# Kernel optimization log

Hardware: AMD Instinct MI355X
Metric: run time of the kernel (lower is better)

The kernel has to match this reference:

```python
import jax, jax.numpy as jnp
import numpy as np

N = 100000   # nodes
E = 1600000  # edges (avg degree 16)
IN = 24
HID = 128
OUT = 12


def setup_inputs() -> dict:
    key = jax.random.key(0)
    ks = jax.random.split(key, 16)
    s = 0.05
    return {
        "inputs": jax.random.normal(ks[0], (N, IN), jnp.float32),
        "src": jax.random.randint(ks[1], (E,), 0, N),
        "dst": jax.random.randint(ks[2], (E,), 0, N),
        "e_w": jax.random.uniform(ks[3], (E, 1), jnp.float32),
        "snorm_n": jax.random.uniform(ks[4], (N, 1), jnp.float32),
        "snorm_e": jax.random.uniform(ks[5], (E, 1), jnp.float32),
        "W_emb": jax.random.normal(ks[6], (IN, HID), jnp.float32) * s,
        "b_emb": jnp.zeros((HID,), jnp.float32),
        "W_self1": jax.random.normal(ks[7], (HID, HID), jnp.float32) * s,
        "W1": jax.random.normal(ks[8], (HID, HID), jnp.float32) * s,
        "b1": jnp.zeros((HID,), jnp.float32),
        "W_self2": jax.random.normal(ks[9], (HID, HID), jnp.float32) * s,
        "W2": jax.random.normal(ks[10], (HID, HID), jnp.float32) * s,
        "b2": jnp.zeros((HID,), jnp.float32),
        "W_fc": jax.random.normal(ks[11], (HID, OUT), jnp.float32) * s,
        "b_fc": jnp.zeros((OUT,), jnp.float32),
    }


def _degrees(src, dst):
    out_deg = jnp.clip(jnp.zeros((N,), jnp.float32).at[src].add(1.0), 1.0)
    in_deg = jnp.clip(jnp.zeros((N,), jnp.float32).at[dst].add(1.0), 1.0)
    return out_deg, in_deg


def _gcn_layer(h, src, dst, e_w, out_deg, in_deg, W_self, W, b):
    # self transform (no bias)
    h_s = h @ W_self
    # source-side symmetric norm, edge-weighted message, sum-aggregate at dst
    feat = h * (out_deg ** -0.5)[:, None]          # [N, H]
    m = feat[src] * e_w                            # [E, H]  u_mul_e
    agg = jax.ops.segment_sum(m, dst, num_segments=N)  # [N, H] sum reduce
    h2 = (agg @ W + b) * (in_deg ** -0.5)[:, None]
    return h_s + h2


def reference(inputs, src, dst, e_w, snorm_n, snorm_e,
              W_emb, b_emb, W_self1, W1, b1, W_self2, W2, b2, W_fc, b_fc):
    out_deg, in_deg = _degrees(src, dst)
    h = inputs @ W_emb + b_emb
    h = jax.nn.relu(_gcn_layer(h, src, dst, e_w, out_deg, in_deg, W_self1, W1, b1))
    h = jax.nn.relu(_gcn_layer(h, src, dst, e_w, out_deg, in_deg, W_self2, W2, b2))
    return h @ W_fc + b_fc
```

## Files before the change

### kernel.cpp

```cpp
#include <hip/hip_runtime.h>

#define NN 100000
#define EE 1600000
#define IN_F 24
#define HID 128
#define OUT_F 12
#define LBLK 128

#define NBKT 782
#define PA_BLKS 512
#define PA_EPB 3125

#define EMB_B 2048
#define PREP_B 264
#define K1_GRID (PA_BLKS + EMB_B + PREP_B)

typedef unsigned char u8;
typedef unsigned short u16;
typedef unsigned int u32;

using short8 = __attribute__((ext_vector_type(8))) short;
using f32x4  = __attribute__((ext_vector_type(4))) float;

__device__ __forceinline__ float bf2f(u16 h) {
  return __uint_as_float(((u32)h) << 16);
}
__device__ __forceinline__ u16 f2bf(float f) {
  u32 u = __float_as_uint(f);
  u32 r = (u + 0x7FFFu + ((u >> 16) & 1u)) >> 16;
  return (u16)r;
}
__device__ __forceinline__ float inv_sqrt_cnt(int c) {
  if (c < 1) c = 1;
  return 1.0f / sqrtf((float)c);
}

__device__ __forceinline__ void emb_body(int eb, const float* __restrict__ inputs,
                                         const float* __restrict__ W_emb,
                                         const float* __restrict__ b_emb,
                                         u16* __restrict__ harr, float* smemW) {
  int t = threadIdx.x;
  float* Wls = smemW;
  float* bls = smemW + IN_F * HID;
  for (int i = t; i < IN_F * HID; i += 256) Wls[i] = W_emb[i];
  if (t < HID) bls[t] = b_emb[t];
  __syncthreads();
  int c = t & 127;
  int sub = t >> 7;
  for (int node = eb * 2 + sub; node < NN; node += EMB_B * 2) {
    const float* xr = inputs + (size_t)node * IN_F;
    float acc = bls[c];
    #pragma unroll
    for (int k = 0; k < IN_F; ++k) acc = fmaf(xr[k], Wls[k * HID + c], acc);
    harr[(size_t)node * HID + c] = f2bf(acc);
  }
}

__device__ __forceinline__ void prep_body(int pb,
    const float* __restrict__ Ws1, const float* __restrict__ W1m,
    const float* __restrict__ Ws2, const float* __restrict__ W2m,
    const float* __restrict__ Wfc,
    u16* __restrict__ WT1, u16* __restrict__ WT2, u16* __restrict__ WfcT) {
  int idx = pb * 256 + (int)threadIdx.x;
  if (idx < 65536) {
    int layer = idx >> 15;
    int rem = idx & 32767;
    int n = rem >> 8, k = rem & 255;
    const float* A = layer ? Ws2 : Ws1;
    const float* B = layer ? W2m : W1m;
    float v = (k < HID) ? A[(size_t)k * HID + n] : B[(size_t)(k - HID) * HID + n];
    (layer ? WT2 : WT1)[(size_t)n * 256 + k] = f2bf(v);
  } else if (idx < 65536 + 2048) {
    int j = idx - 65536;
    int n = j >> 7, k = j & 127;
    WfcT[(size_t)n * 128 + k] = f2bf(n < OUT_F ? Wfc[(size_t)k * OUT_F + n] : 0.f);
  }
}

__global__ __launch_bounds__(256) void k1(
    const int* __restrict__ src, const int* __restrict__ dst,
    u32* __restrict__ histgD, u32* __restrict__ histgS,
    const float* __restrict__ inputs, const float* __restrict__ W_emb,
    const float* __restrict__ b_emb, u16* __restrict__ harr,
    const float* __restrict__ Ws1, const float* __restrict__ W1m,
    const float* __restrict__ Ws2, const float* __restrict__ W2m,
    const float* __restrict__ Wfc,
    u16* __restrict__ WT1, u16* __restrict__ WT2, u16* __restrict__ WfcT) {
  __shared__ __align__(16) char sm[13312];
  int b = blockIdx.x, t = threadIdx.x;
  if (b < PA_BLKS) {
    u32* histD = (u32*)sm;
    u32* histS = histD + 1024;
    for (int i = t; i < 2048; i += 256) histD[i] = 0;
    __syncthreads();
    int e0 = b * PA_EPB;
    for (int e = e0 + t; e < e0 + PA_EPB; e += 256) {
      atomicAdd(&histD[dst[e] >> 7], 1u);
      atomicAdd(&histS[src[e] >> 7], 1u);
    }
    __syncthreads();
    for (int i = t; i < 1024; i += 256) {
      histgD[(size_t)b * 1024 + i] = histD[i];
      histgS[(size_t)b * 1024 + i] = histS[i];
    }
  } else if (b < PA_BLKS + EMB_B) {
    emb_body(b - PA_BLKS, inputs, W_emb, b_emb, harr, (float*)sm);
  } else {
    prep_body(b - PA_BLKS - EMB_B, Ws1, W1m, Ws2, W2m, Wfc, WT1, WT2, WfcT);
  }
}

__global__ __launch_bounds__(256) void k_scan1(u32* __restrict__ histgD,
                                               u32* __restrict__ histgS,
                                               u32* __restrict__ totalsD,
                                               u32* __restrict__ totalsS) {
  __shared__ u32 s[512];
  int b = blockIdx.x, t = threadIdx.x;
  u32* hist = (b < NBKT) ? histgD : histgS;
  u32* tot  = (b < NBKT) ? totalsD : totalsS;
  int k = (b < NBKT) ? b : b - NBKT;
  u32 v0 = hist[(size_t)t * 1024 + k];
  u32 v1 = hist[(size_t)(t + 256) * 1024 + k];
  s[t] = v0; s[t + 256] = v1;
  __syncthreads();
  for (int off = 1; off < 512; off <<= 1) {
    u32 a0 = (t >= off) ? s[t - off] : 0;
    u32 a1 = (t + 256 >= off) ? s[t + 256 - off] : 0;
    __syncthreads();
    s[t] += a0; s[t + 256] += a1;
    __syncthreads();
  }
  hist[(size_t)t * 1024 + k] = s[t] - v0;
  hist[(size_t)(t + 256) * 1024 + k] = s[t + 256] - v1;
  if (t == 255) tot[k] = s[511];
}

__global__ __launch_bounds__(1024) void k_scan2(const u32* __restrict__ totalsD,
                                                const u32* __restrict__ totalsS,
                                                u32* __restrict__ estartD,
                                                u32* __restrict__ sstart) {
  __shared__ u32 s[1024];
  const u32* tot = blockIdx.x ? totalsS : totalsD;
  u32* est       = blockIdx.x ? sstart  : estartD;
  int t = threadIdx.x;
  u32 v = (t < NBKT) ? tot[t] : 0;
  s[t] = v;
  __syncthreads();
  for (int off = 1; off < 1024; off <<= 1) {
    u32 a = (t >= off) ? s[t - off] : 0;
    __syncthreads();
    s[t] += a;
    __syncthreads();
  }
  if (t < NBKT) est[t] = s[t] - v;
  if (t == NBKT - 1) est[NBKT] = s[t];
}

__global__ __launch_bounds__(256) void k_passbS(
    const int* __restrict__ src, const u32* __restrict__ histgS,
    const u32* __restrict__ sstart, u8* __restrict__ lo8) {
  __shared__ u32 cur[1024];
  int pb = blockIdx.x, t = threadIdx.x;
  for (int i = t; i < 1024; i += 256)
    cur[i] = ((i < NBKT) ? sstart[i] : 0u) + histgS[(size_t)pb * 1024 + i];
  __syncthreads();
  int e0 = pb * PA_EPB;
  for (int e = e0 + t; e < e0 + PA_EPB; e += 256) {
    int s = src[e];
    u32 pos = atomicAdd(&cur[s >> 7], 1u);
    lo8[pos] = (u8)(s & 127);
  }
}

__global__ __launch_bounds__(256) void k_countS(const u8* __restrict__ lo8,
                                                const u32* __restrict__ sstart,
                                                float* __restrict__ out_norm) {
  __shared__ u32 cnt[128];
  int k = blockIdx.x, t = threadIdx.x;
  if (t < 128) cnt[t] = 0;
  __syncthreads();
  int e0 = (int)sstart[k], e1 = (int)sstart[k + 1];
  for (int e = e0 + t; e < e1; e += 256) atomicAdd(&cnt[lo8[e]], 1u);
  __syncthreads();
  if (t < 128) {
    int node = k * 128 + t;
    if (node < NN) out_norm[node] = inv_sqrt_cnt((int)cnt[t]);
  }
}

__global__ __launch_bounds__(256) void k_passbD(
    const int* __restrict__ src, const int* __restrict__ dst,
    const float* __restrict__ e_w, const float* __restrict__ out_norm,
    const u32* __restrict__ histgD, const u32* __restrict__ estartD,
    u32* __restrict__ csr_stage, u8* __restrict__ dl8) {
  __shared__ u32 cur[1024];
  int pb = blockIdx.x, t = threadIdx.x;
  for (int i = t; i < 1024; i += 256)
    cur[i] = ((i < NBKT) ? estartD[i] : 0u) + histgD[(size_t)pb * 1024 + i];
  __syncthreads();
  int e0 = pb * PA_EPB;
  for (int e = e0 + t; e < e0 + PA_EPB; e += 256) {
    int s = src[e], d = dst[e];
    float w = e_w[e] * out_norm[s];
    u32 pos = atomicAdd(&cur[d >> 7], 1u);
    csr_stage[pos] = (((u32)f2bf(w)) << 17) | (u32)s;
    dl8[pos] = (u8)(d & 127);
  }
}

__global__ __launch_bounds__(256) void k_reorder(
    const u32* __restrict__ csr_stage, const u8* __restrict__ dl8,
    const u32* __restrict__ estart, u32* __restrict__ csr,
    int* __restrict__ row_start, float* __restrict__ in_norm) {
  __shared__ u32 cnt[128], pfx[128], cur[128];
  int k = blockIdx.x, t = threadIdx.x;
  if (t < 128) cnt[t] = 0;
  __syncthreads();
  int e0 = (int)estart[k], e1 = (int)estart[k + 1];
  for (int e = e0 + t; e < e1; e += 256) atomicAdd(&cnt[dl8[e]], 1u);
  __syncthreads();
  if (t < 128) pfx[t] = cnt[t];
  __syncthreads();
  for (int off = 1; off < 128; off <<= 1) {
    u32 v = (t < 128 && t >= off) ? pfx[t - off] : 0;
    __syncthreads();
    if (t < 128) pfx[t] += v;
    __syncthreads();
  }
  if (t < 128) {
    u32 start = (u32)e0 + pfx[t] - cnt[t];
    cur[t] = start;
    int node = k * 128 + t;
    if (node < NN) {
      row_start[node] = (int)start;
      in_norm[node] = inv_sqrt_cnt((int)cnt[t]);
    }
  }
  if (k == NBKT - 1 && t == 0) row_start[NN] = e1;
  __syncthreads();
  for (int e = e0 + t; e < e1; e += 256) {
    u32 pos = atomicAdd(&cur[dl8[e]], 1u);
    csr[pos] = csr_stage[e];
  }
}

__global__ __launch_bounds__(256) void k_agg(const u16* __restrict__ harr,
                                             const int* __restrict__ row_start,
                                             const float* __restrict__ in_norm,
                                             const u32* __restrict__ csr,
                                             u16* __restrict__ aggr) {
  int t = threadIdx.x;
  int node = blockIdx.x * 8 + (t >> 5);
  if (node >= NN) return;
  int lane = t & 31;
  int s0 = row_start[node], s1 = row_start[node + 1];
  float ax = 0.f, ay = 0.f, az = 0.f, aw = 0.f;
  for (int i0 = s0; i0 < s1; i0 += 32) {
    u32 pk = 0;
    if (i0 + lane < s1) pk = csr[i0 + lane];
    int m = s1 - i0; if (m > 32) m = 32;
    int j = 0;
    for (; j + 4 <= m; j += 4) {
      u32 p0 = __shfl(pk, j,     32);
      u32 p1 = __shfl(pk, j + 1, 32);
      u32 p2 = __shfl(pk, j + 2, 32);
      u32 p3 = __shfl(pk, j + 3, 32);
      ushort4 h0 = *(const ushort4*)(harr + (size_t)(p0 & 0x1FFFF) * HID + lane * 4);
      ushort4 h1 = *(const ushort4*)(harr + (size_t)(p1 & 0x1FFFF) * HID + lane * 4);
      ushort4 h2 = *(const ushort4*)(harr + (size_t)(p2 & 0x1FFFF) * HID + lane * 4);
      ushort4 h3 = *(const ushort4*)(harr + (size_t)(p3 & 0x1FFFF) * HID + lane * 4);
      float w0 = bf2f((u16)(p0 >> 17));
      float w1 = bf2f((u16)(p1 >> 17));
      float w2 = bf2f((u16)(p2 >> 17));
      float w3 = bf2f((u16)(p3 >> 17));
      ax = fmaf(w0, bf2f(h0.x), ax); ay = fmaf(w0, bf2f(h0.y), ay);
      az = fmaf(w0, bf2f(h0.z), az); aw = fmaf(w0, bf2f(h0.w), aw);
      ax = fmaf(w1, bf2f(h1.x), ax); ay = fmaf(w1, bf2f(h1.y), ay);
      az = fmaf(w1, bf2f(h1.z), az); aw = fmaf(w1, bf2f(h1.w), aw);
      ax = fmaf(w2, bf2f(h2.x), ax); ay = fmaf(w2, bf2f(h2.y), ay);
      az = fmaf(w2, bf2f(h2.z), az); aw = fmaf(w2, bf2f(h2.w), aw);
      ax = fmaf(w3, bf2f(h3.x), ax); ay = fmaf(w3, bf2f(h3.y), ay);
      az = fmaf(w3, bf2f(h3.z), az); aw = fmaf(w3, bf2f(h3.w), aw);
    }
    for (; j < m; ++j) {
      u32 p = __shfl(pk, j, 32);
      float w = bf2f((u16)(p >> 17));
      ushort4 hv = *(const ushort4*)(harr + (size_t)(p & 0x1FFFF) * HID + lane * 4);
      ax = fmaf(w, bf2f(hv.x), ax); ay = fmaf(w, bf2f(hv.y), ay);
      az = fmaf(w, bf2f(hv.z), az); aw = fmaf(w, bf2f(hv.w), aw);
    }
  }
  float inn = in_norm[node];
  ushort4 r;
  r.x = f2bf(ax * inn); r.y = f2bf(ay * inn);
  r.z = f2bf(az * inn); r.w = f2bf(aw * inn);
  *(ushort4*)(aggr + (size_t)node * HID + lane * 4) = r;
}

template<int FC>
__global__ __launch_bounds__(512) void k_layer(u16* __restrict__ harr,
    const u16* __restrict__ aggr,
    const u16* __restrict__ WT, const float* __restrict__ bias,
    const float* __restrict__ in_norm,
    const u16* __restrict__ WfcT, const float* __restrict__ b_fc,
    float* __restrict__ out) {
  __shared__ char smem[135168];
  const int t = threadIdx.x;
  const int r0 = blockIdx.x * LBLK;

  #pragma unroll
  for (int i = 0; i < 4; ++i) {
    int boff = i * 8192 + t * 16;
    int row = boff >> 8, col = boff & 255;
    uint4 v = *(const uint4*)(harr + (size_t)(r0 + row) * HID + (col >> 1));
    *(uint4*)(smem + row * 512 + (col ^ ((row & 7) << 4))) = v;
  }
  #pragma unroll
  for (int i = 0; i < 4; ++i) {
    int boff = i * 8192 + t * 16;
    int row = boff >> 8, col = boff & 255;
    uint4 v = *(const uint4*)(aggr + (size_t)(r0 + row) * HID + (col >> 1));
    *(uint4*)(smem + row * 512 + (256 + (col ^ ((row & 7) << 4)))) = v;
  }
  #pragma unroll
  for (int i = 0; i < 8; ++i) {
    int boff = i * 8192 + t * 16;
    int row = boff >> 9, col = boff & 511;
    uint4 v = *(const uint4*)(WT + (size_t)row * 256 + (col >> 1));
    *(uint4*)(smem + 65536 + row * 512 + (col ^ ((row & 7) << 4))) = v;
  }
  if (FC && t < 256) {
    int row = t >> 4, col = (t & 15) * 16;
    uint4 v = *(const uint4*)(WfcT + (size_t)row * 128 + (col >> 1));
    *(uint4*)(smem + 131072 + row * 256 + (col ^ ((row & 7) << 4))) = v;
  }
  __syncthreads();

  const int lane = t & 63, w = t >> 6;
  const int l15 = lane & 15, lhi = lane >> 4;

  f32x4 acc[8];
  #pragma unroll
  for (int nf = 0; nf < 8; ++nf) acc[nf] = (f32x4){0.f, 0.f, 0.f, 0.f};

  const int arow = w * 16 + l15;
  const char* pa = smem + arow * 512;
  const int aswz = (arow & 7) << 4;
  #pragma unroll
  for (int ks = 0; ks < 8; ++ks) {
    int kb = ks * 64 + (lhi << 4);
    short8 a = *(const short8*)(pa + (kb ^ aswz));
    #pragma unroll
    for (int nf = 0; nf < 8; ++nf) {
      int brow = nf * 16 + l15;
      short8 bf = *(const short8*)(smem + 65536 + brow * 512 + (kb ^ ((brow & 7) << 4)));
      acc[nf] = __builtin_amdgcn_mfma_f32_16x16x32_bf16(a, bf, acc[nf], 0, 0, 0);
    }
  }

  float bcol[8];
  #pragma unroll
  for (int nf = 0; nf < 8; ++nf) bcol[nf] = bias[nf * 16 + l15];

  if (!FC) {
    #pragma unroll
    for (int r = 0; r < 4; ++r) {
      int grow = r0 + w * 16 + (lhi << 2) + r;
      if (grow < NN) {
        float inn = in_norm[grow];
        #pragma unroll
        for (int nf = 0; nf < 8; ++nf) {
          float v = acc[nf][r] + inn * bcol[nf];
          harr[(size_t)grow * HID + nf * 16 + l15] = f2bf(fmaxf(v, 0.f));
        }
      }
    }
  } else {
    #pragma unroll
    for (int r = 0; r < 4; ++r) {
      int lrow = w * 16 + (lhi << 2) + r;
      int grow = r0 + lrow;
      float inn = (grow < NN) ? in_norm[grow] : 0.f;
      #pragma unroll
      for (int nf = 0; nf < 8; ++nf) {
        int col = nf * 16 + l15;
        float v = fmaxf(acc[nf][r] + inn * bcol[nf], 0.f);
        *(u16*)(smem + lrow * 256 + ((col * 2) ^ ((lrow & 7) << 4))) = f2bf(v);
      }
    }
    __syncthreads();
    f32x4 a2 = (f32x4){0.f, 0.f, 0.f, 0.f};
    const char* pa2 = smem + (w * 16 + l15) * 256;
    const int as2 = (l15 & 7) << 4;
    #pragma unroll
    for (int ks = 0; ks < 4; ++ks) {
      int kb = ks * 64 + (lhi << 4);
      short8 a = *(const short8*)(pa2 + (kb ^ as2));
      short8 bf = *(const short8*)(smem + 131072 + l15 * 256 + (kb ^ as2));
      a2 = __builtin_amdgcn_mfma_f32_16x16x32_bf16(a, bf, a2, 0, 0, 0);
    }
    if (l15 < OUT_F) {
      float bo = b_fc[l15];
      #pragma unroll
      for (int r = 0; r < 4; ++r) {
        int grow = r0 + w * 16 + (lhi << 2) + r;
        if (grow < NN) out[(size_t)grow * OUT_F + l15] = a2[r] + bo;
      }
    }
  }
}

extern "C" void kernel_launch(void* const* d_in, const int* in_sizes, int n_in,
                              void* d_out, int out_size, void* d_ws, size_t ws_size,
                              hipStream_t stream) {
  (void)in_sizes; (void)n_in; (void)out_size;
  const float* inputs  = (const float*)d_in[0];
  const int*   src     = (const int*)d_in[1];
  const int*   dst     = (const int*)d_in[2];
  const float* e_w     = (const float*)d_in[3];
  const float* W_emb   = (const float*)d_in[6];
  const float* b_emb   = (const float*)d_in[7];
  const float* W_self1 = (const float*)d_in[8];
  const float* W1      = (const float*)d_in[9];
  const float* b1      = (const float*)d_in[10];
  const float* W_self2 = (const float*)d_in[11];
  const float* W2      = (const float*)d_in[12];
  const float* b2      = (const float*)d_in[13];
  const float* W_fc    = (const float*)d_in[14];
  const float* b_fc    = (const float*)d_in[15];
  float* out = (float*)d_out;

  u32* histgD      = (u32*)d_ws;
  u32* histgS      = histgD + (size_t)512 * 1024;
  u32* totalsD     = histgS + (size_t)512 * 1024;
  u32* estartD     = totalsD + 1024;
  u32* totalsS     = estartD + 1024;
  u32* sstart      = totalsS + 1024;
  float* out_norm  = (float*)(sstart + 1024);
  float* in_norm   = out_norm + NN;
  int* row_start   = (int*)(in_norm + NN);
  u8* lo8          = (u8*)(row_start + NN + 4);
  u32* csr_stage   = (u32*)(lo8 + EE);
  u32* csr         = csr_stage + EE;
  u16* harr        = (u16*)(csr + EE);
  u16* aggr        = harr + (size_t)NN * HID;
  u16* WT1         = aggr + (size_t)NN * HID;
  u16* WT2         = WT1 + 32768;
  u16* WfcT        = WT2 + 32768;

  const size_t NEED = (size_t)2 * 512 * 1024 * 4 + 4096 * 4 + (size_t)(3 * NN + 4) * 4
                      + (size_t)EE * 9 + (size_t)NN * HID * 4 + (2 * 32768 + 2048) * 2;
  if (ws_size < NEED) return;

  hipLaunchKernelGGL(k1, dim3(K1_GRID), dim3(256), 0, stream,
                     src, dst, histgD, histgS, inputs, W_emb, b_emb, harr,
                     W_self1, W1, W_self2, W2, W_fc, WT1, WT2, WfcT);
  hipLaunchKernelGGL(k_scan1, dim3(2 * NBKT), dim3(256), 0, stream,
                     histgD, histgS, totalsD, totalsS);
  hipLaunchKernelGGL(k_scan2, dim3(2), dim3(1024), 0, stream,
                     totalsD, totalsS, estartD, sstart);
  hipLaunchKernelGGL(k_passbS, dim3(PA_BLKS), dim3(256), 0, stream,
                     src, histgS, sstart, lo8);
  hipLaunchKernelGGL(k_countS, dim3(NBKT), dim3(256), 0, stream, lo8, sstart, out_norm);
  hipLaunchKernelGGL(k_passbD, dim3(PA_BLKS), dim3(256), 0, stream,
                     src, dst, e_w, out_norm, histgD, estartD, csr_stage, lo8);
  hipLaunchKernelGGL(k_reorder, dim3(NBKT), dim3(256), 0, stream,
                     csr_stage, lo8, estartD, csr, row_start, in_norm);
  hipLaunchKernelGGL(k_agg, dim3((NN + 7) / 8), dim3(256), 0, stream,
                     harr, row_start, in_norm, csr, aggr);
  hipLaunchKernelGGL(k_layer<0>, dim3((NN + LBLK - 1) / LBLK), dim3(512), 0, stream,
                     harr, aggr, WT1, b1, in_norm, WfcT, b_fc, out);
  hipLaunchKernelGGL(k_agg, dim3((NN + 7) / 8), dim3(256), 0, stream,
                     harr, row_start, in_norm, csr, aggr);
  hipLaunchKernelGGL(k_layer<1>, dim3((NN + LBLK - 1) / LBLK), dim3(512), 0, stream,
                     harr, aggr, WT2, b2, in_norm, WfcT, b_fc, out);
}
```

Before: 352.8 us.

## Merge src/dst bucket passes and widen aggregation loads to 16 bytes

The separate source and destination bucketing passes become one kernel that reads src/dst once and scatters into both bucket arrays. Because out_norm is no longer known during bucketing, the out-degree norm is applied later in the aggregation kernel, where each edge weight is rescaled on load. The aggregation kernel now has each half-warp load 8 bf16 values (16 bytes) per lane and handle alternating edges, combining the halves with a shuffle at the end. This saves a launch and a pass over the edge arrays, at the cost of extra norm gathers and bf16 re-rounding in both aggregation calls. It also adds a barrier in the layer kernel and reuses the csr buffer as temporary space for the source bytes.

```diff
diff --git a/kernel.cpp b/kernel.cpp
--- a/kernel.cpp
+++ b/kernel.cpp
@@ -30,6 +30,8 @@
   u32 r = (u + 0x7FFFu + ((u >> 16) & 1u)) >> 16;
   return (u16)r;
 }
+__device__ __forceinline__ float bflo(u32 p) { return __uint_as_float(p << 16); }
+__device__ __forceinline__ float bfhi(u32 p) { return __uint_as_float(p & 0xFFFF0000u); }
 __device__ __forceinline__ float inv_sqrt_cnt(int c) {
   if (c < 1) c = 1;
   return 1.0f / sqrtf((float)c);
@@ -156,23 +158,31 @@
   if (t == NBKT - 1) est[NBKT] = s[t];
 }
 
-__global__ __launch_bounds__(256) void k_passbS(
-    const int* __restrict__ src, const u32* __restrict__ histgS,
-    const u32* __restrict__ sstart, u8* __restrict__ lo8) {
-  __shared__ u32 cur[1024];
+__global__ __launch_bounds__(256) void k_passb(
+    const int* __restrict__ src, const int* __restrict__ dst,
+    const float* __restrict__ e_w,
+    const u32* __restrict__ histgD, const u32* __restrict__ estartD,
+    const u32* __restrict__ histgS, const u32* __restrict__ sstart,
+    u32* __restrict__ csr_stage, u8* __restrict__ dl8, u8* __restrict__ sl8) {
+  __shared__ u32 curD[1024], curS[1024];
   int pb = blockIdx.x, t = threadIdx.x;
-  for (int i = t; i < 1024; i += 256)
-    cur[i] = ((i < NBKT) ? sstart[i] : 0u) + histgS[(size_t)pb * 1024 + i];
+  for (int i = t; i < 1024; i += 256) {
+    curD[i] = ((i < NBKT) ? estartD[i] : 0u) + histgD[(size_t)pb * 1024 + i];
+    curS[i] = ((i < NBKT) ? sstart[i] : 0u) + histgS[(size_t)pb * 1024 + i];
+  }
   __syncthreads();
   int e0 = pb * PA_EPB;
   for (int e = e0 + t; e < e0 + PA_EPB; e += 256) {
-    int s = src[e];
-    u32 pos = atomicAdd(&cur[s >> 7], 1u);
-    lo8[pos] = (u8)(s & 127);
-  }
-}
-
-__global__ __launch_bounds__(256) void k_countS(const u8* __restrict__ lo8,
+    int s = src[e], d = dst[e];
+    u32 posS = atomicAdd(&curS[s >> 7], 1u);
+    sl8[posS] = (u8)(s & 127);
+    u32 posD = atomicAdd(&curD[d >> 7], 1u);
+    csr_stage[posD] = (((u32)f2bf(e_w[e])) << 17) | (u32)s;
+    dl8[posD] = (u8)(d & 127);
+  }
+}
+
+__global__ __launch_bounds__(256) void k_countS(const u8* __restrict__ sl8,
                                                 const u32* __restrict__ sstart,
                                                 float* __restrict__ out_norm) {
   __shared__ u32 cnt[128];
@@ -180,31 +190,11 @@
   if (t < 128) cnt[t] = 0;
   __syncthreads();
   int e0 = (int)sstart[k], e1 = (int)sstart[k + 1];
-  for (int e = e0 + t; e < e1; e += 256) atomicAdd(&cnt[lo8[e]], 1u);
+  for (int e = e0 + t; e < e1; e += 256) atomicAdd(&cnt[sl8[e]], 1u);
   __syncthreads();
   if (t < 128) {
     int node = k * 128 + t;
     if (node < NN) out_norm[node] = inv_sqrt_cnt((int)cnt[t]);
-  }
-}
-
-__global__ __launch_bounds__(256) void k_passbD(
-    const int* __restrict__ src, const int* __restrict__ dst,
-    const float* __restrict__ e_w, const float* __restrict__ out_norm,
-    const u32* __restrict__ histgD, const u32* __restrict__ estartD,
-    u32* __restrict__ csr_stage, u8* __restrict__ dl8) {
-  __shared__ u32 cur[1024];
-  int pb = blockIdx.x, t = threadIdx.x;
-  for (int i = t; i < 1024; i += 256)
-    cur[i] = ((i < NBKT) ? estartD[i] : 0u) + histgD[(size_t)pb * 1024 + i];
-  __syncthreads();
-  int e0 = pb * PA_EPB;
-  for (int e = e0 + t; e < e0 + PA_EPB; e += 256) {
-    int s = src[e], d = dst[e];
-    float w = e_w[e] * out_norm[s];
-    u32 pos = atomicAdd(&cur[d >> 7], 1u);
-    csr_stage[pos] = (((u32)f2bf(w)) << 17) | (u32)s;
-    dl8[pos] = (u8)(d & 127);
   }
 }
 
@@ -247,54 +237,72 @@
 __global__ __launch_bounds__(256) void k_agg(const u16* __restrict__ harr,
                                              const int* __restrict__ row_start,
                                              const float* __restrict__ in_norm,
+                                             const float* __restrict__ out_norm,
                                              const u32* __restrict__ csr,
                                              u16* __restrict__ aggr) {
   int t = threadIdx.x;
   int node = blockIdx.x * 8 + (t >> 5);
   if (node >= NN) return;
   int lane = t & 31;
+  int half = lane >> 4;
+  int li = lane & 15;
   int s0 = row_start[node], s1 = row_start[node + 1];
-  float ax = 0.f, ay = 0.f, az = 0.f, aw = 0.f;
+  float acc[8] = {0.f, 0.f, 0.f, 0.f, 0.f, 0.f, 0.f, 0.f};
   for (int i0 = s0; i0 < s1; i0 += 32) {
-    u32 pk = 0;
-    if (i0 + lane < s1) pk = csr[i0 + lane];
+    u32 pk2 = 0;
+    if (i0 + lane < s1) {
+      u32 pk = csr[i0 + lane];
+      u32 sv = pk & 0x1FFFF;
+      float w = bf2f((u16)(pk >> 17)) * out_norm[sv];
+      pk2 = (((u32)f2bf(w)) << 17) | sv;
+    }
     int m = s1 - i0; if (m > 32) m = 32;
-    int j = 0;
-    for (; j + 4 <= m; j += 4) {
-      u32 p0 = __shfl(pk, j,     32);
-      u32 p1 = __shfl(pk, j + 1, 32);
-      u32 p2 = __shfl(pk, j + 2, 32);
-      u32 p3 = __shfl(pk, j + 3, 32);
-      ushort4 h0 = *(const ushort4*)(harr + (size_t)(p0 & 0x1FFFF) * HID + lane * 4);
-      ushort4 h1 = *(const ushort4*)(harr + (size_t)(p1 & 0x1FFFF) * HID + lane * 4);
-      ushort4 h2 = *(const ushort4*)(harr + (size_t)(p2 & 0x1FFFF) * HID + lane * 4);
-      ushort4 h3 = *(const ushort4*)(harr + (size_t)(p3 & 0x1FFFF) * HID + lane * 4);
-      float w0 = bf2f((u16)(p0 >> 17));
-      float w1 = bf2f((u16)(p1 >> 17));
-      float w2 = bf2f((u16)(p2 >> 17));
-      float w3 = bf2f((u16)(p3 >> 17));
-      ax = fmaf(w0, bf2f(h0.x), ax); ay = fmaf(w0, bf2f(h0.y), ay);
-      az = fmaf(w0, bf2f(h0.z), az); aw = fmaf(w0, bf2f(h0.w), aw);
-      ax = fmaf(w1, bf2f(h1.x), ax); ay = fmaf(w1, bf2f(h1.y), ay);
-      az = fmaf(w1, bf2f(h1.z), az); aw = fmaf(w1, bf2f(h1.w), aw);
-      ax = fmaf(w2, bf2f(h2.x), ax); ay = fmaf(w2, bf2f(h2.y), ay);
-      az = fmaf(w2, bf2f(h2.z), az); aw = fmaf(w2, bf2f(h2.w), aw);
-      ax = fmaf(w3, bf2f(h3.x), ax); ay = fmaf(w3, bf2f(h3.y), ay);
-      az = fmaf(w3, bf2f(h3.z), az); aw = fmaf(w3, bf2f(h3.w), aw);
-    }
-    for (; j < m; ++j) {
-      u32 p = __shfl(pk, j, 32);
-      float w = bf2f((u16)(p >> 17));
-      ushort4 hv = *(const ushort4*)(harr + (size_t)(p & 0x1FFFF) * HID + lane * 4);
-      ax = fmaf(w, bf2f(hv.x), ax); ay = fmaf(w, bf2f(hv.y), ay);
-      az = fmaf(w, bf2f(hv.z), az); aw = fmaf(w, bf2f(hv.w), aw);
-    }
-  }
-  float inn = in_norm[node];
-  ushort4 r;
-  r.x = f2bf(ax * inn); r.y = f2bf(ay * inn);
-  r.z = f2bf(az * inn); r.w = f2bf(aw * inn);
-  *(ushort4*)(aggr + (size_t)node * HID + lane * 4) = r;
+    int jj = 0;
+    for (; jj + 8 <= m; jj += 8) {
+      uint4 hv[4]; float wq[4];
+      #pragma unroll
+      for (int q = 0; q < 4; ++q) {
+        u32 p = __shfl(pk2, jj + 2 * q + half, 32);
+        wq[q] = bf2f((u16)(p >> 17));
+        hv[q] = *(const uint4*)(harr + (size_t)(p & 0x1FFFF) * HID + li * 8);
+      }
+      #pragma unroll
+      for (int q = 0; q < 4; ++q) {
+        acc[0] = fmaf(wq[q], bflo(hv[q].x), acc[0]);
+        acc[1] = fmaf(wq[q], bfhi(hv[q].x), acc[1]);
+        acc[2] = fmaf(wq[q], bflo(hv[q].y), acc[2]);
+        acc[3] = fmaf(wq[q], bfhi(hv[q].y), acc[3]);
+        acc[4] = fmaf(wq[q], bflo(hv[q].z), acc[4]);
+        acc[5] = fmaf(wq[q], bfhi(hv[q].z), acc[5]);
+        acc[6] = fmaf(wq[q], bflo(hv[q].w), acc[6]);
+        acc[7] = fmaf(wq[q], bfhi(hv[q].w), acc[7]);
+      }
+    }
+    for (; jj < m; jj += 2) {
+      int idx = jj + half;
+      int sidx = (idx < m) ? idx : m - 1;
+      u32 p = __shfl(pk2, sidx, 32);
+      float w = (idx < m) ? bf2f((u16)(p >> 17)) : 0.f;
+      uint4 hv = *(const uint4*)(harr + (size_t)(p & 0x1FFFF) * HID + li * 8);
+      acc[0] = fmaf(w, bflo(hv.x), acc[0]);
+      acc[1] = fmaf(w, bfhi(hv.x), acc[1]);
+      acc[2] = fmaf(w, bflo(hv.y), acc[2]);
+      acc[3] = fmaf(w, bfhi(hv.y), acc[3]);
+      acc[4] = fmaf(w, bflo(hv.z), acc[4]);
+      acc[5] = fmaf(w, bfhi(hv.z), acc[5]);
+      acc[6] = fmaf(w, bflo(hv.w), acc[6]);
+      acc[7] = fmaf(w, bfhi(hv.w), acc[7]);
+    }
+  }
+  #pragma unroll
+  for (int q = 0; q < 8; ++q) acc[q] += __shfl_xor(acc[q], 16, 32);
+  if (half == 0) {
+    float inn = in_norm[node];
+    union { u16 h[8]; uint4 v; } pk;
+    #pragma unroll
+    for (int x = 0; x < 8; ++x) pk.h[x] = f2bf(acc[x] * inn);
+    *(uint4*)(aggr + (size_t)node * HID + li * 8) = pk.v;
+  }
 }
 
 template<int FC>
@@ -376,6 +384,7 @@
       }
     }
   } else {
+    __syncthreads();
     #pragma unroll
     for (int r = 0; r < 4; ++r) {
       int lrow = w * 16 + (lhi << 2) + r;
@@ -439,9 +448,10 @@
   float* out_norm  = (float*)(sstart + 1024);
   float* in_norm   = out_norm + NN;
   int* row_start   = (int*)(in_norm + NN);
-  u8* lo8          = (u8*)(row_start + NN + 4);
-  u32* csr_stage   = (u32*)(lo8 + EE);
+  u8* dl8          = (u8*)(row_start + NN + 4);
+  u32* csr_stage   = (u32*)(dl8 + EE);
   u32* csr         = csr_stage + EE;
+  u8* sl8          = (u8*)csr;
   u16* harr        = (u16*)(csr + EE);
   u16* aggr        = harr + (size_t)NN * HID;
   u16* WT1         = aggr + (size_t)NN * HID;
@@ -459,19 +469,18 @@
                      histgD, histgS, totalsD, totalsS);
   hipLaunchKernelGGL(k_scan2, dim3(2), dim3(1024), 0, stream,
                      totalsD, totalsS, estartD, sstart);
-  hipLaunchKernelGGL(k_passbS, dim3(PA_BLKS), dim3(256), 0, stream,
-                     src, histgS, sstart, lo8);
-  hipLaunchKernelGGL(k_countS, dim3(NBKT), dim3(256), 0, stream, lo8, sstart, out_norm);
-  hipLaunchKernelGGL(k_passbD, dim3(PA_BLKS), dim3(256), 0, stream,
-                     src, dst, e_w, out_norm, histgD, estartD, csr_stage, lo8);
+  hipLaunchKernelGGL(k_passb, dim3(PA_BLKS), dim3(256), 0, stream,
+                     src, dst, e_w, histgD, estartD, histgS, sstart,
+                     csr_stage, dl8, sl8);
+  hipLaunchKernelGGL(k_countS, dim3(NBKT), dim3(256), 0, stream, sl8, sstart, out_norm);
   hipLaunchKernelGGL(k_reorder, dim3(NBKT), dim3(256), 0, stream,
-                     csr_stage, lo8, estartD, csr, row_start, in_norm);
+                     csr_stage, dl8, estartD, csr, row_start, in_norm);
   hipLaunchKernelGGL(k_agg, dim3((NN + 7) / 8), dim3(256), 0, stream,
-                     harr, row_start, in_norm, csr, aggr);
+                     harr, row_start, in_norm, out_norm, csr, aggr);
   hipLaunchKernelGGL(k_layer<0>, dim3((NN + LBLK - 1) / LBLK), dim3(512), 0, stream,
                      harr, aggr, WT1, b1, in_norm, WfcT, b_fc, out);
   hipLaunchKernelGGL(k_agg, dim3((NN + 7) / 8), dim3(256), 0, stream,
-                     harr, row_start, in_norm, csr, aggr);
+                     harr, row_start, in_norm, out_norm, csr, aggr);
   hipLaunchKernelGGL(k_layer<1>, dim3((NN + LBLK - 1) / LBLK), dim3(512), 0, stream,
                      harr, aggr, WT2, b2, in_norm, WfcT, b_fc, out);
 }
```

Measured after the change: 364.0 us. 1.03x slower.

## Replace source-side bucket sort with windowed shared-memory out-degree histogram

Applied to the files above, without the earlier changes.

Out-degree is now computed by a windowed LDS histogram over source IDs (packed 16-bit counters, 64 partial copies per window, then reduced), replacing the source-side scatter and count passes. The destination bucket sort now writes one 64-bit record per edge (src, local dst, raw edge weight), and reorder sorts in place through a shared-memory staging buffer, removing the separate dl8 and csr_stage arrays. Multiplying the weight by the source norm moves into the aggregation kernel, so that work is repeated in both layers. The staging buffer is capped at RCAP edges per bucket, and a bucket with more edges would silently drop them.

```diff
diff --git a/kernel.cpp b/kernel.cpp
--- a/kernel.cpp
+++ b/kernel.cpp
@@ -8,8 +8,16 @@
 #define LBLK 128
 
 #define NBKT 782
-#define PA_BLKS 512
-#define PA_EPB 3125
+#define PA_BLKS 256
+#define PA_EPB 6250
+
+#define OW_BITS 15
+#define OWIN 32768
+#define OW_GRP 4
+#define OW_CPY 64
+#define OW_EPB 25000
+
+#define RCAP 2560
 
 #define EMB_B 2048
 #define PREP_B 264
@@ -18,6 +26,7 @@
 typedef unsigned char u8;
 typedef unsigned short u16;
 typedef unsigned int u32;
+typedef unsigned long long u64;
 
 using short8 = __attribute__((ext_vector_type(8))) short;
 using f32x4  = __attribute__((ext_vector_type(4))) float;
@@ -33,6 +42,41 @@
 __device__ __forceinline__ float inv_sqrt_cnt(int c) {
   if (c < 1) c = 1;
   return 1.0f / sqrtf((float)c);
+}
+
+__global__ __launch_bounds__(256) void k_odeg(const int* __restrict__ src,
+                                              u32* __restrict__ whist) {
+  __shared__ u32 hist[OWIN / 2];
+  int b = blockIdx.x, t = threadIdx.x;
+  int g = b >> 6, sb = b & 63;
+  for (int i = t; i < OWIN / 2; i += 256) hist[i] = 0;
+  __syncthreads();
+  int e0 = sb * OW_EPB;
+  for (int e = e0 + t; e < e0 + OW_EPB; e += 256) {
+    int s = src[e];
+    if ((s >> OW_BITS) == g) {
+      int i = s & (OWIN - 1);
+      atomicAdd(&hist[i >> 1], (i & 1) ? 0x10000u : 1u);
+    }
+  }
+  __syncthreads();
+  u32* out = whist + (size_t)b * (OWIN / 2);
+  for (int i = t; i < OWIN / 2; i += 256) out[i] = hist[i];
+}
+
+__global__ __launch_bounds__(256) void k_onorm(const u32* __restrict__ whist,
+                                               float* __restrict__ out_norm) {
+  int i = blockIdx.x * 256 + (int)threadIdx.x;
+  if (i >= NN / 2) return;
+  int n0 = 2 * i;
+  int g = n0 >> OW_BITS;
+  int pi = (n0 & (OWIN - 1)) >> 1;
+  const u32* base = whist + (size_t)(g * OW_CPY) * (OWIN / 2) + pi;
+  u32 s = 0;
+  #pragma unroll 8
+  for (int c = 0; c < OW_CPY; ++c) s += base[(size_t)c * (OWIN / 2)];
+  out_norm[n0]     = inv_sqrt_cnt((int)(s & 0xFFFFu));
+  out_norm[n0 + 1] = inv_sqrt_cnt((int)(s >> 16));
 }
 
 __device__ __forceinline__ void emb_body(int eb, const float* __restrict__ inputs,
@@ -78,8 +122,7 @@
 }
 
 __global__ __launch_bounds__(256) void k1(
-    const int* __restrict__ src, const int* __restrict__ dst,
-    u32* __restrict__ histgD, u32* __restrict__ histgS,
+    const int* __restrict__ dst, u32* __restrict__ histgD,
     const float* __restrict__ inputs, const float* __restrict__ W_emb,
     const float* __restrict__ b_emb, u16* __restrict__ harr,
     const float* __restrict__ Ws1, const float* __restrict__ W1m,
@@ -90,19 +133,13 @@
   int b = blockIdx.x, t = threadIdx.x;
   if (b < PA_BLKS) {
     u32* histD = (u32*)sm;
-    u32* histS = histD + 1024;
-    for (int i = t; i < 2048; i += 256) histD[i] = 0;
+    for (int i = t; i < 1024; i += 256) histD[i] = 0;
     __syncthreads();
     int e0 = b * PA_EPB;
-    for (int e = e0 + t; e < e0 + PA_EPB; e += 256) {
+    for (int e = e0 + t; e < e0 + PA_EPB; e += 256)
       atomicAdd(&histD[dst[e] >> 7], 1u);
-      atomicAdd(&histS[src[e] >> 7], 1u);
-    }
-    __syncthreads();
-    for (int i = t; i < 1024; i += 256) {
-      histgD[(size_t)b * 1024 + i] = histD[i];
-      histgS[(size_t)b * 1024 + i] = histS[i];
-    }
+    __syncthreads();
+    for (int i = t; i < 1024; i += 256) histgD[(size_t)b * 1024 + i] = histD[i];
   } else if (b < PA_BLKS + EMB_B) {
     emb_body(b - PA_BLKS, inputs, W_emb, b_emb, harr, (float*)sm);
   } else {
@@ -111,39 +148,27 @@
 }
 
 __global__ __launch_bounds__(256) void k_scan1(u32* __restrict__ histgD,
-                                               u32* __restrict__ histgS,
-                                               u32* __restrict__ totalsD,
-                                               u32* __restrict__ totalsS) {
-  __shared__ u32 s[512];
-  int b = blockIdx.x, t = threadIdx.x;
-  u32* hist = (b < NBKT) ? histgD : histgS;
-  u32* tot  = (b < NBKT) ? totalsD : totalsS;
-  int k = (b < NBKT) ? b : b - NBKT;
-  u32 v0 = hist[(size_t)t * 1024 + k];
-  u32 v1 = hist[(size_t)(t + 256) * 1024 + k];
-  s[t] = v0; s[t + 256] = v1;
-  __syncthreads();
-  for (int off = 1; off < 512; off <<= 1) {
-    u32 a0 = (t >= off) ? s[t - off] : 0;
-    u32 a1 = (t + 256 >= off) ? s[t + 256 - off] : 0;
-    __syncthreads();
-    s[t] += a0; s[t + 256] += a1;
-    __syncthreads();
-  }
-  hist[(size_t)t * 1024 + k] = s[t] - v0;
-  hist[(size_t)(t + 256) * 1024 + k] = s[t + 256] - v1;
-  if (t == 255) tot[k] = s[511];
+                                               u32* __restrict__ totalsD) {
+  __shared__ u32 s[256];
+  int k = blockIdx.x, t = threadIdx.x;
+  u32 v = histgD[(size_t)t * 1024 + k];
+  s[t] = v;
+  __syncthreads();
+  for (int off = 1; off < 256; off <<= 1) {
+    u32 a = (t >= off) ? s[t - off] : 0;
+    __syncthreads();
+    s[t] += a;
+    __syncthreads();
+  }
+  histgD[(size_t)t * 1024 + k] = s[t] - v;
+  if (t == 255) totalsD[k] = s[255];
 }
 
 __global__ __launch_bounds__(1024) void k_scan2(const u32* __restrict__ totalsD,
-                                                const u32* __restrict__ totalsS,
-                                                u32* __restrict__ estartD,
-                                                u32* __restrict__ sstart) {
+                                                u32* __restrict__ estartD) {
   __shared__ u32 s[1024];
-  const u32* tot = blockIdx.x ? totalsS : totalsD;
-  u32* est       = blockIdx.x ? sstart  : estartD;
   int t = threadIdx.x;
-  u32 v = (t < NBKT) ? tot[t] : 0;
+  u32 v = (t < NBKT) ? totalsD[t] : 0;
   s[t] = v;
   __syncthreads();
   for (int off = 1; off < 1024; off <<= 1) {
@@ -152,47 +177,15 @@
     s[t] += a;
     __syncthreads();
   }
-  if (t < NBKT) est[t] = s[t] - v;
-  if (t == NBKT - 1) est[NBKT] = s[t];
-}
-
-__global__ __launch_bounds__(256) void k_passbS(
-    const int* __restrict__ src, const u32* __restrict__ histgS,
-    const u32* __restrict__ sstart, u8* __restrict__ lo8) {
-  __shared__ u32 cur[1024];
-  int pb = blockIdx.x, t = threadIdx.x;
-  for (int i = t; i < 1024; i += 256)
-    cur[i] = ((i < NBKT) ? sstart[i] : 0u) + histgS[(size_t)pb * 1024 + i];
-  __syncthreads();
-  int e0 = pb * PA_EPB;
-  for (int e = e0 + t; e < e0 + PA_EPB; e += 256) {
-    int s = src[e];
-    u32 pos = atomicAdd(&cur[s >> 7], 1u);
-    lo8[pos] = (u8)(s & 127);
-  }
-}
-
-__global__ __launch_bounds__(256) void k_countS(const u8* __restrict__ lo8,
-                                                const u32* __restrict__ sstart,
-                                                float* __restrict__ out_norm) {
-  __shared__ u32 cnt[128];
-  int k = blockIdx.x, t = threadIdx.x;
-  if (t < 128) cnt[t] = 0;
-  __syncthreads();
-  int e0 = (int)sstart[k], e1 = (int)sstart[k + 1];
-  for (int e = e0 + t; e < e1; e += 256) atomicAdd(&cnt[lo8[e]], 1u);
-  __syncthreads();
-  if (t < 128) {
-    int node = k * 128 + t;
-    if (node < NN) out_norm[node] = inv_sqrt_cnt((int)cnt[t]);
-  }
-}
-
-__global__ __launch_bounds__(256) void k_passbD(
+  if (t < NBKT) estartD[t] = s[t] - v;
+  if (t == NBKT - 1) estartD[NBKT] = s[t];
+}
+
+__global__ __launch_bounds__(256) void k_passb(
     const int* __restrict__ src, const int* __restrict__ dst,
-    const float* __restrict__ e_w, const float* __restrict__ out_norm,
+    const float* __restrict__ e_w,
     const u32* __restrict__ histgD, const u32* __restrict__ estartD,
-    u32* __restrict__ csr_stage, u8* __restrict__ dl8) {
+    u64* __restrict__ ebuf) {
   __shared__ u32 cur[1024];
   int pb = blockIdx.x, t = threadIdx.x;
   for (int i = t; i < 1024; i += 256)
@@ -201,23 +194,28 @@
   int e0 = pb * PA_EPB;
   for (int e = e0 + t; e < e0 + PA_EPB; e += 256) {
     int s = src[e], d = dst[e];
-    float w = e_w[e] * out_norm[s];
+    u32 hi = (u32)s | (((u32)(d & 127)) << 17);
+    u64 rec = ((u64)hi << 32) | (u64)__float_as_uint(e_w[e]);
     u32 pos = atomicAdd(&cur[d >> 7], 1u);
-    csr_stage[pos] = (((u32)f2bf(w)) << 17) | (u32)s;
-    dl8[pos] = (u8)(d & 127);
+    ebuf[pos] = rec;
   }
 }
 
 __global__ __launch_bounds__(256) void k_reorder(
-    const u32* __restrict__ csr_stage, const u8* __restrict__ dl8,
-    const u32* __restrict__ estart, u32* __restrict__ csr,
+    u64* __restrict__ ebuf, const u32* __restrict__ estart,
     int* __restrict__ row_start, float* __restrict__ in_norm) {
+  __shared__ u64 stage[RCAP];
   __shared__ u32 cnt[128], pfx[128], cur[128];
   int k = blockIdx.x, t = threadIdx.x;
   if (t < 128) cnt[t] = 0;
   __syncthreads();
   int e0 = (int)estart[k], e1 = (int)estart[k + 1];
-  for (int e = e0 + t; e < e1; e += 256) atomicAdd(&cnt[dl8[e]], 1u);
+  int n = e1 - e0; if (n > RCAP) n = RCAP;
+  for (int i = t; i < n; i += 256) {
+    u64 v = ebuf[e0 + i];
+    stage[i] = v;
+    atomicAdd(&cnt[(u32)(v >> 49) & 127], 1u);
+  }
   __syncthreads();
   if (t < 128) pfx[t] = cnt[t];
   __syncthreads();
@@ -238,16 +236,18 @@
   }
   if (k == NBKT - 1 && t == 0) row_start[NN] = e1;
   __syncthreads();
-  for (int e = e0 + t; e < e1; e += 256) {
-    u32 pos = atomicAdd(&cur[dl8[e]], 1u);
-    csr[pos] = csr_stage[e];
+  for (int i = t; i < n; i += 256) {
+    u64 v = stage[i];
+    u32 pos = atomicAdd(&cur[(u32)(v >> 49) & 127], 1u);
+    ebuf[pos] = v;
   }
 }
 
 __global__ __launch_bounds__(256) void k_agg(const u16* __restrict__ harr,
                                              const int* __restrict__ row_start,
                                              const float* __restrict__ in_norm,
-                                             const u32* __restrict__ csr,
+                                             const float* __restrict__ out_norm,
+                                             const u64* __restrict__ ebuf,
                                              u16* __restrict__ aggr) {
   int t = threadIdx.x;
   int node = blockIdx.x * 8 + (t >> 5);
@@ -256,15 +256,20 @@
   int s0 = row_start[node], s1 = row_start[node + 1];
   float ax = 0.f, ay = 0.f, az = 0.f, aw = 0.f;
   for (int i0 = s0; i0 < s1; i0 += 32) {
-    u32 pk = 0;
-    if (i0 + lane < s1) pk = csr[i0 + lane];
+    u32 pk2 = 0;
+    if (i0 + lane < s1) {
+      u64 rec = ebuf[i0 + lane];
+      u32 sv = (u32)(rec >> 32) & 0x1FFFF;
+      float w = __uint_as_float((u32)rec) * out_norm[sv];
+      pk2 = (((u32)f2bf(w)) << 17) | sv;
+    }
     int m = s1 - i0; if (m > 32) m = 32;
     int j = 0;
     for (; j + 4 <= m; j += 4) {
-      u32 p0 = __shfl(pk, j,     32);
-      u32 p1 = __shfl(pk, j + 1, 32);
-      u32 p2 = __shfl(pk, j + 2, 32);
-      u32 p3 = __shfl(pk, j + 3, 32);
+      u32 p0 = __shfl(pk2, j,     32);
+      u32 p1 = __shfl(pk2, j + 1, 32);
+      u32 p2 = __shfl(pk2, j + 2, 32);
+      u32 p3 = __shfl(pk2, j + 3, 32);
       ushort4 h0 = *(const ushort4*)(harr + (size_t)(p0 & 0x1FFFF) * HID + lane * 4);
       ushort4 h1 = *(const ushort4*)(harr + (size_t)(p1 & 0x1FFFF) * HID + lane * 4);
       ushort4 h2 = *(const ushort4*)(harr + (size_t)(p2 & 0x1FFFF) * HID + lane * 4);
@@ -283,7 +288,7 @@
       az = fmaf(w3, bf2f(h3.z), az); aw = fmaf(w3, bf2f(h3.w), aw);
     }
     for (; j < m; ++j) {
-      u32 p = __shfl(pk, j, 32);
+      u32 p = __shfl(pk2, j, 32);
       float w = bf2f((u16)(p >> 17));
       ushort4 hv = *(const ushort4*)(harr + (size_t)(p & 0x1FFFF) * HID + lane * 4);
       ax = fmaf(w, bf2f(hv.x), ax); ay = fmaf(w, bf2f(hv.y), ay);
@@ -376,6 +381,7 @@
       }
     }
   } else {
+    __syncthreads();
     #pragma unroll
     for (int r = 0; r < 4; ++r) {
       int lrow = w * 16 + (lhi << 2) + r;
@@ -431,47 +437,41 @@
   float* out = (float*)d_out;
 
   u32* histgD      = (u32*)d_ws;
-  u32* histgS      = histgD + (size_t)512 * 1024;
-  u32* totalsD     = histgS + (size_t)512 * 1024;
+  u32* totalsD     = histgD + (size_t)PA_BLKS * 1024;
   u32* estartD     = totalsD + 1024;
-  u32* totalsS     = estartD + 1024;
-  u32* sstart      = totalsS + 1024;
-  float* out_norm  = (float*)(sstart + 1024);
+  float* out_norm  = (float*)(estartD + 1024);
   float* in_norm   = out_norm + NN;
   int* row_start   = (int*)(in_norm + NN);
-  u8* lo8          = (u8*)(row_start + NN + 4);
-  u32* csr_stage   = (u32*)(lo8 + EE);
-  u32* csr         = csr_stage + EE;
-  u16* harr        = (u16*)(csr + EE);
+  u64* ebuf        = (u64*)(row_start + NN + 4);
+  u16* harr        = (u16*)(ebuf + EE);
   u16* aggr        = harr + (size_t)NN * HID;
   u16* WT1         = aggr + (size_t)NN * HID;
   u16* WT2         = WT1 + 32768;
   u16* WfcT        = WT2 + 32768;
-
-  const size_t NEED = (size_t)2 * 512 * 1024 * 4 + 4096 * 4 + (size_t)(3 * NN + 4) * 4
-                      + (size_t)EE * 9 + (size_t)NN * HID * 4 + (2 * 32768 + 2048) * 2;
+  u32* whist       = (u32*)ebuf;
+
+  const size_t NEED = (size_t)PA_BLKS * 1024 * 4 + 2048 * 4 + (size_t)(3 * NN + 4) * 4
+                      + (size_t)EE * 8 + (size_t)NN * HID * 4 + (2 * 32768 + 2048) * 2;
   if (ws_size < NEED) return;
 
+  hipLaunchKernelGGL(k_odeg, dim3(OW_GRP * OW_CPY), dim3(256), 0, stream, src, whist);
+  hipLaunchKernelGGL(k_onorm, dim3((NN / 2 + 255) / 256), dim3(256), 0, stream,
+                     whist, out_norm);
   hipLaunchKernelGGL(k1, dim3(K1_GRID), dim3(256), 0, stream,
-                     src, dst, histgD, histgS, inputs, W_emb, b_emb, harr,
+                     dst, histgD, inputs, W_emb, b_emb, harr,
                      W_self1, W1, W_self2, W2, W_fc, WT1, WT2, WfcT);
-  hipLaunchKernelGGL(k_scan1, dim3(2 * NBKT), dim3(256), 0, stream,
-                     histgD, histgS, totalsD, totalsS);
-  hipLaunchKernelGGL(k_scan2, dim3(2), dim3(1024), 0, stream,
-                     totalsD, totalsS, estartD, sstart);
-  hipLaunchKernelGGL(k_passbS, dim3(PA_BLKS), dim3(256), 0, stream,
-                     src, histgS, sstart, lo8);
-  hipLaunchKernelGGL(k_countS, dim3(NBKT), dim3(256), 0, stream, lo8, sstart, out_norm);
-  hipLaunchKernelGGL(k_passbD, dim3(PA_BLKS), dim3(256), 0, stream,
-                     src, dst, e_w, out_norm, histgD, estartD, csr_stage, lo8);
+  hipLaunchKernelGGL(k_scan1, dim3(NBKT), dim3(256), 0, stream, histgD, totalsD);
+  hipLaunchKernelGGL(k_scan2, dim3(1), dim3(1024), 0, stream, totalsD, estartD);
+  hipLaunchKernelGGL(k_passb, dim3(PA_BLKS), dim3(256), 0, stream,
+                     src, dst, e_w, histgD, estartD, ebuf);
   hipLaunchKernelGGL(k_reorder, dim3(NBKT), dim3(256), 0, stream,
-                     csr_stage, lo8, estartD, csr, row_start, in_norm);
+                     ebuf, estartD, row_start, in_norm);
   hipLaunchKernelGGL(k_agg, dim3((NN + 7) / 8), dim3(256), 0, stream,
-                     harr, row_start, in_norm, csr, aggr);
+                     harr, row_start, in_norm, out_norm, ebuf, aggr);
   hipLaunchKernelGGL(k_layer<0>, dim3((NN + LBLK - 1) / LBLK), dim3(512), 0, stream,
                      harr, aggr, WT1, b1, in_norm, WfcT, b_fc, out);
   hipLaunchKernelGGL(k_agg, dim3((NN + 7) / 8), dim3(256), 0, stream,
-                     harr, row_start, in_norm, csr, aggr);
+                     harr, row_start, in_norm, out_norm, ebuf, aggr);
   hipLaunchKernelGGL(k_layer<1>, dim3((NN + LBLK - 1) / LBLK), dim3(512), 0, stream,
                      harr, aggr, WT2, b2, in_norm, WfcT, b_fc, out);
 }
```

New measurement: 349.6 us. Within noise of the previous version (-0.9%).
